# Kernel optimization log

Hardware: AMD Instinct MI355X
Metric: run time of the kernel (lower is better)

Reference implementation:

```python
import jax, jax.numpy as jnp
import numpy as np

N = 100000   # nodes
E = 3200000  # edges (avg degree 32)
D = 128      # in_channels
H = 128      # hidden_channels
A, S, ETH = 3, 2, 3  # head output dims


def _w(k, o, i):
    return jax.random.normal(k, (o, i), dtype=jnp.float32) / np.sqrt(i).astype(np.float32)


def setup_inputs() -> dict:
    key = jax.random.key(0)
    ks = jax.random.split(key, 20)
    x = jax.random.normal(ks[0], (N, D), dtype=jnp.float32)
    edge_index = jax.random.randint(ks[1], (2, E), 0, N, dtype=jnp.int64)
    inp = {"x": x, "edge_index": edge_index}
    # SAGEConv params: Wl applied to mean-aggregated neighbors, Wr to root, plus bias
    dims = [("1", D, H), ("2", H, H), ("3", H, H), ("a", H, A), ("s", H, S), ("e", H, ETH)]
    ki = 2
    for tag, i, o in dims:
        inp[f"W{tag}l"] = _w(ks[ki], o, i); ki += 1
        inp[f"W{tag}r"] = _w(ks[ki], o, i); ki += 1
        inp[f"b{tag}"] = jnp.zeros((o,), dtype=jnp.float32)
    return inp


def _sage(x, src, dst, inv_deg, Wl, Wr, b):
    # mean aggregation of source features onto destination nodes, then linear
    agg = jax.ops.segment_sum(x[src], dst, num_segments=N) * inv_deg  # [N, d]
    return agg @ Wl.T + x @ Wr.T + b


def reference(x, edge_index,
              W1l, W1r, b1, W2l, W2r, b2, W3l, W3r, b3,
              Wal, War, ba, Wsl, Wsr, bs, Wel, Wer, be):
    src, dst = edge_index[0], edge_index[1]
    deg = jax.ops.segment_sum(jnp.ones((E,), jnp.float32), dst, num_segments=N)
    inv_deg = (1.0 / jnp.maximum(deg, 1.0))[:, None]  # [N,1]
    h = jax.nn.relu(_sage(x, src, dst, inv_deg, W1l, W1r, b1))
    h = jax.nn.relu(_sage(h, src, dst, inv_deg, W2l, W2r, b2))
    h = jax.nn.relu(_sage(h, src, dst, inv_deg, W3l, W3r, b3))
    age_out = _sage(h, src, dst, inv_deg, Wal, War, ba)
    sex_out = _sage(h, src, dst, inv_deg, Wsl, Wsr, bs)
    eth_out = _sage(h, src, dst, inv_deg, Wel, Wer, be)
    return (age_out, sex_out, eth_out)
```

## Files before the change

kernel.cpp:

```cpp
#include <hip/hip_runtime.h>

#define TPB 256
#define NB1 256
#define NBUCK 512

using half4_t = __attribute__((ext_vector_type(4))) _Float16;
using half8_t = __attribute__((ext_vector_type(8))) _Float16;
using f32x4 = __attribute__((ext_vector_type(4))) float;


__global__ __launch_bounds__(256) void hist1_k(const int* __restrict__ ei,
                                               int* __restrict__ hist, int E, int stripe) {
  __shared__ int h[NBUCK];
  for (int i = threadIdx.x; i < NBUCK; i += 256) h[i] = 0;
  __syncthreads();
  int b0 = blockIdx.x * stripe;
  int b1 = min(b0 + stripe, E);
  for (int e = b0 + threadIdx.x; e < b1; e += 256) atomicAdd(&h[ei[E + e] >> 8], 1);
  __syncthreads();
  for (int i = threadIdx.x; i < NBUCK; i += 256) hist[i * NB1 + blockIdx.x] = h[i];
}

__global__ void scan1_k(const int* __restrict__ src, int* __restrict__ out,
                        int* __restrict__ chunk, int n) {
  __shared__ int sh[TPB];
  int i = blockIdx.x * TPB + threadIdx.x;
  int v = (i < n) ? src[i] : 0;
  sh[threadIdx.x] = v;
  __syncthreads();
  for (int off = 1; off < TPB; off <<= 1) {
    int t = (threadIdx.x >= off) ? sh[threadIdx.x - off] : 0;
    __syncthreads();
    sh[threadIdx.x] += t;
    __syncthreads();
  }
  if (i < n) out[i] = sh[threadIdx.x] - v;
  if (threadIdx.x == TPB - 1) chunk[blockIdx.x] = sh[TPB - 1];
}

__global__ void scan2_k(int* __restrict__ chunk, int nb) {
  __shared__ int sh[512];
  int v = (threadIdx.x < nb) ? chunk[threadIdx.x] : 0;
  sh[threadIdx.x] = v;
  __syncthreads();
  for (int off = 1; off < 512; off <<= 1) {
    int t = (threadIdx.x >= off) ? sh[threadIdx.x - off] : 0;
    __syncthreads();
    sh[threadIdx.x] += t;
    __syncthreads();
  }
  if (threadIdx.x < nb) chunk[threadIdx.x] = sh[threadIdx.x] - v;
}

__global__ void scan3_k(int* __restrict__ out, const int* __restrict__ chunk, int n) {
  int i = blockIdx.x * TPB + threadIdx.x;
  if (i < n) out[i] += chunk[blockIdx.x];
}

__global__ __launch_bounds__(256) void scatter1_k(const int* __restrict__ ei,
                                                  const int* __restrict__ base,
                                                  unsigned* __restrict__ ebuf, int E,
                                                  int stripe) {
  __shared__ int cur[NBUCK];
  for (int i = threadIdx.x; i < NBUCK; i += 256) cur[i] = base[i * NB1 + blockIdx.x];
  __syncthreads();
  int b0 = blockIdx.x * stripe;
  int b1 = min(b0 + stripe, E);
  for (int e = b0 + threadIdx.x; e < b1; e += 256) {
    int s = ei[e];
    int d = ei[E + e];
    int p = atomicAdd(&cur[d >> 8], 1);
    ebuf[p] = (unsigned)s | ((unsigned)(d & 255) << 24);
  }
}

__global__ __launch_bounds__(256) void build_k(const unsigned* __restrict__ ebuf,
                                               const int* __restrict__ base,
                                               int* __restrict__ row_start,
                                               int* __restrict__ deg,
                                               float* __restrict__ invd,
                                               int* __restrict__ csr, int N, int E) {
  __shared__ int h[256];
  __shared__ int excl[256];
  __shared__ int bse[2];
  int b = blockIdx.x;
  int t = threadIdx.x;
  if (t == 0) {
    bse[0] = base[b * NB1];
    bse[1] = (b + 1 < NBUCK) ? base[(b + 1) * NB1] : E;
  }
  h[t] = 0;
  __syncthreads();
  int bs = bse[0], be = bse[1];
  for (int e = bs + t; e < be; e += 256) atomicAdd(&h[ebuf[e] >> 24], 1);
  __syncthreads();
  int v = h[t];
  excl[t] = v;
  __syncthreads();
  for (int off = 1; off < 256; off <<= 1) {
    int tv = (t >= off) ? excl[t - off] : 0;
    __syncthreads();
    excl[t] += tv;
    __syncthreads();
  }
  int ex = excl[t] - v;
  int node = b * 256 + t;
  if (node < N) {
    row_start[node] = bs + ex;
    deg[node] = v;
    invd[node] = 1.0f / fmaxf((float)v, 1.0f);
  }
  h[t] = bs + ex;
  __syncthreads();
  for (int e = bs + t; e < be; e += 256) {
    unsigned p = ebuf[e];
    int pos = atomicAdd(&h[p >> 24], 1);
    csr[pos] = (int)(p & 0xFFFFFFu);
  }
}


__global__ void f2h_k(const float* __restrict__ in, _Float16* __restrict__ out, int n4) {
  int i = blockIdx.x * TPB + threadIdx.x;
  if (i < n4) {
    float4 v = ((const float4*)in)[i];
    half4_t o;
    o.x = (_Float16)v.x; o.y = (_Float16)v.y; o.z = (_Float16)v.z; o.w = (_Float16)v.w;
    ((half4_t*)out)[i] = o;
  }
}

__global__ void w6_k(const float* __restrict__ w0, const float* __restrict__ w1,
                     const float* __restrict__ w2, const float* __restrict__ w3,
                     const float* __restrict__ w4, const float* __restrict__ w5,
                     _Float16* __restrict__ out) {
  int t = blockIdx.x * TPB + threadIdx.x;
  if (t >= 6 * 4096) return;
  int which = t >> 12, i = t & 4095;
  const float* src = which == 0 ? w0 : which == 1 ? w1 : which == 2 ? w2
                   : which == 3 ? w3 : which == 4 ? w4 : w5;
  float4 v = ((const float4*)src)[i];
  half4_t o;
  o.x = (_Float16)v.x; o.y = (_Float16)v.y; o.z = (_Float16)v.z; o.w = (_Float16)v.w;
  ((half4_t*)out)[(size_t)which * 4096 + i] = o;
}


__global__ __launch_bounds__(256) void agg128_k(const _Float16* __restrict__ hb,
                                                const int* __restrict__ csr,
                                                const int* __restrict__ row_start,
                                                const int* __restrict__ deg,
                                                const float* __restrict__ invd,
                                                _Float16* __restrict__ out, int n) {
  int node = (blockIdx.x << 2) + (threadIdx.x >> 6);
  if (node >= n) return;
  int lane = threadIdx.x & 63;
  int g = lane >> 4;
  int l = lane & 15;
  int s = row_start[node];
  int c = deg[node];
  const _Float16* base = hb + (l << 3);
  float a0 = 0.f, a1 = 0.f, a2 = 0.f, a3 = 0.f;
  float a4 = 0.f, a5 = 0.f, a6 = 0.f, a7 = 0.f;
  int j = 0;
  if (c >= 16) {
    int id[4];
#pragma unroll
    for (int p = 0; p < 4; ++p) id[p] = csr[s + 4 * p + g];
    while (true) {
      half8_t v[4];
#pragma unroll
      for (int p = 0; p < 4; ++p) v[p] = *(const half8_t*)&base[(size_t)id[p] * 128];
      j += 16;
      bool more = (j + 16 <= c);
      if (more) {
#pragma unroll
        for (int p = 0; p < 4; ++p) id[p] = csr[s + j + 4 * p + g];
      }
#pragma unroll
      for (int p = 0; p < 4; ++p) {
        a0 += (float)v[p][0]; a1 += (float)v[p][1];
        a2 += (float)v[p][2]; a3 += (float)v[p][3];
        a4 += (float)v[p][4]; a5 += (float)v[p][5];
        a6 += (float)v[p][6]; a7 += (float)v[p][7];
      }
      if (!more) break;
    }
  }
  if (j < c) {
    int cm1 = c - 1;
#pragma unroll
    for (int p = 0; p < 4; ++p) {
      int e = j + 4 * p + g;
      float m = (e < c) ? 1.f : 0.f;
      int id = csr[s + min(e, cm1)];
      half8_t v = *(const half8_t*)&base[(size_t)id * 128];
      a0 = fmaf(m, (float)v[0], a0); a1 = fmaf(m, (float)v[1], a1);
      a2 = fmaf(m, (float)v[2], a2); a3 = fmaf(m, (float)v[3], a3);
      a4 = fmaf(m, (float)v[4], a4); a5 = fmaf(m, (float)v[5], a5);
      a6 = fmaf(m, (float)v[6], a6); a7 = fmaf(m, (float)v[7], a7);
    }
  }
  a0 += __shfl_xor(a0, 16); a1 += __shfl_xor(a1, 16);
  a2 += __shfl_xor(a2, 16); a3 += __shfl_xor(a3, 16);
  a4 += __shfl_xor(a4, 16); a5 += __shfl_xor(a5, 16);
  a6 += __shfl_xor(a6, 16); a7 += __shfl_xor(a7, 16);
  a0 += __shfl_xor(a0, 32); a1 += __shfl_xor(a1, 32);
  a2 += __shfl_xor(a2, 32); a3 += __shfl_xor(a3, 32);
  a4 += __shfl_xor(a4, 32); a5 += __shfl_xor(a5, 32);
  a6 += __shfl_xor(a6, 32); a7 += __shfl_xor(a7, 32);
  if (g == 0) {
    float w = invd[node];
    half8_t r;
    r[0] = (_Float16)(a0 * w); r[1] = (_Float16)(a1 * w);
    r[2] = (_Float16)(a2 * w); r[3] = (_Float16)(a3 * w);
    r[4] = (_Float16)(a4 * w); r[5] = (_Float16)(a5 * w);
    r[6] = (_Float16)(a6 * w); r[7] = (_Float16)(a7 * w);
    *(half8_t*)&out[(size_t)node * 128 + (l << 3)] = r;
  }
}


__global__ __launch_bounds__(256) void gemm2_k(
    const _Float16* __restrict__ Aagg, const _Float16* __restrict__ Ah,
    const _Float16* __restrict__ Wh,
    const float* __restrict__ bias, _Float16* __restrict__ outh, int n, int do_relu) {
  int wave = threadIdx.x >> 6;
  int lane = threadIdx.x & 63;
  int quad = lane >> 4;
  int l16 = lane & 15;
  int m0 = blockIdx.x * 64 + wave * 16;
  int arow = m0 + l16;
  bool valid = arow < n;
  size_t abase = (size_t)arow * 128 + quad * 8;

  f32x4 acc[8];
#pragma unroll
  for (int c = 0; c < 8; ++c) acc[c] = (f32x4){0.f, 0.f, 0.f, 0.f};

#pragma unroll
  for (int s = 0; s < 2; ++s) {
    const _Float16* A = s ? Ah : Aagg;
    const _Float16* W = Wh + (size_t)s * 16384;
#pragma unroll
    for (int kb = 0; kb < 128; kb += 32) {
      half8_t af;
      if (valid) {
        af = *(const half8_t*)&A[abase + kb];
      } else {
#pragma unroll
        for (int jj = 0; jj < 8; ++jj) af[jj] = (_Float16)0;
      }
#pragma unroll
      for (int c = 0; c < 8; ++c) {
        half8_t bf = *(const half8_t*)&W[(size_t)(c * 16 + l16) * 128 + kb + quad * 8];
        acc[c] = __builtin_amdgcn_mfma_f32_16x16x32_f16(af, bf, acc[c], 0, 0, 0);
      }
    }
  }

#pragma unroll
  for (int c = 0; c < 8; ++c) {
    float bcol = bias[c * 16 + l16];
#pragma unroll
    for (int r = 0; r < 4; ++r) {
      int row = m0 + quad * 4 + r;
      if (row < n) {
        float v = acc[c][r] + bcol;
        if (do_relu) v = fmaxf(v, 0.f);
        outh[(size_t)row * 128 + c * 16 + l16] = (_Float16)v;
      }
    }
  }
}


__global__ void pack_head_k(const float* __restrict__ Wal, const float* __restrict__ War,
                            const float* __restrict__ ba, const float* __restrict__ Wsl,
                            const float* __restrict__ Wsr, const float* __restrict__ bsx,
                            const float* __restrict__ Wel, const float* __restrict__ Wer,
                            const float* __restrict__ be, _Float16* __restrict__ Wcat,
                            float* __restrict__ bcat) {
  int t = blockIdx.x * TPB + threadIdx.x;
  float v = 0.f;
  bool ok = t < 2048;
  if (t < 384) v = Wal[t];
  else if (t < 640) v = Wsl[t - 384];
  else if (t < 1024) v = Wel[t - 640];
  else if (t < 1408) v = War[t - 1024];
  else if (t < 1664) v = Wsr[t - 1408];
  else if (t < 2048) v = Wer[t - 1664];
  if (ok) Wcat[t] = (_Float16)v;
  if (t < 16) {
    float b = 0.f;
    if (t >= 8 && t < 11) b = ba[t - 8];
    else if (t >= 11 && t < 13) b = bsx[t - 11];
    else if (t >= 13) b = be[t - 13];
    bcat[t] = b;
  }
}


__global__ __launch_bounds__(256) void head_gemm_k(const _Float16* __restrict__ h,
                                                   const _Float16* __restrict__ Wcat,
                                                   const float* __restrict__ bcat,
                                                   float* __restrict__ out_lr, int n) {
  __shared__ float hs[64 * 132];
  __shared__ float Ws[16 * 128];
  __shared__ float bsh[16];
  int tid = threadIdx.x;
  int m0 = blockIdx.x * 64;
  {
    half8_t w = *(const half8_t*)&Wcat[tid * 8];
#pragma unroll
    for (int jj = 0; jj < 8; ++jj) Ws[tid * 8 + jj] = (float)w[jj];
    if (tid < 16) bsh[tid] = bcat[tid];
  }
  {
    int row = tid >> 2, q = tid & 3;
    int grow = m0 + row;
#pragma unroll
    for (int j = 0; j < 4; ++j) {
      half8_t v;
      if (grow < n) {
        v = *(const half8_t*)&h[(size_t)grow * 128 + q * 32 + j * 8];
      } else {
#pragma unroll
        for (int jj = 0; jj < 8; ++jj) v[jj] = (_Float16)0;
      }
#pragma unroll
      for (int jj = 0; jj < 8; ++jj) hs[row * 132 + q * 32 + j * 8 + jj] = (float)v[jj];
    }
  }
  __syncthreads();
  int row = tid & 63, og = tid >> 6;
  float acc[4] = {0.f, 0.f, 0.f, 0.f};
#pragma unroll
  for (int k4 = 0; k4 < 32; ++k4) {
    float4 hv = *(float4*)&hs[row * 132 + k4 * 4];
#pragma unroll
    for (int i = 0; i < 4; ++i) {
      float4 wv = *(float4*)&Ws[(og * 4 + i) * 128 + k4 * 4];
      acc[i] += hv.x * wv.x + hv.y * wv.y + hv.z * wv.z + hv.w * wv.w;
    }
  }
  int grow = m0 + row;
  if (grow < n) {
#pragma unroll
    for (int i = 0; i < 4; ++i)
      out_lr[(size_t)grow * 16 + og * 4 + i] = acc[i] + bsh[og * 4 + i];
  }
}


__global__ void agg8_k(const float* __restrict__ hlr, const int* __restrict__ csr,
                       const int* __restrict__ row_start, const int* __restrict__ deg,
                       const float* __restrict__ invd, float* __restrict__ out, int n) {
  int node = (blockIdx.x << 2) + (threadIdx.x >> 6);
  if (node >= n) return;
  int lane = threadIdx.x & 63;
  int c2 = lane & 3;
  int g = lane >> 2;
  int s = row_start[node], cnt = deg[node];
  float ax = 0.f, ay = 0.f;
  int j = 0;
  for (; j + 32 <= cnt; j += 32) {
#pragma unroll
    for (int p = 0; p < 2; ++p) {
      int id = csr[s + j + 16 * p + g];
      float2 v = *(const float2*)&hlr[(size_t)id * 16 + 2 * c2];
      ax += v.x;
      ay += v.y;
    }
  }
  if (j < cnt) {
    int cm1 = cnt - 1;
#pragma unroll
    for (int p = 0; p < 2; ++p) {
      int e = j + 16 * p + g;
      float m = (e < cnt) ? 1.f : 0.f;
      int id = csr[s + min(e, cm1)];
      float2 v = *(const float2*)&hlr[(size_t)id * 16 + 2 * c2];
      ax = fmaf(m, v.x, ax);
      ay = fmaf(m, v.y, ay);
    }
  }
  ax += __shfl_xor(ax, 4);  ay += __shfl_xor(ay, 4);
  ax += __shfl_xor(ax, 8);  ay += __shfl_xor(ay, 8);
  ax += __shfl_xor(ax, 16); ay += __shfl_xor(ay, 16);
  ax += __shfl_xor(ax, 32); ay += __shfl_xor(ay, 32);
  if (g == 0) {
    float w = invd[node];
    float r0 = ax * w + hlr[(size_t)node * 16 + 8 + 2 * c2];
    float r1 = ay * w + hlr[(size_t)node * 16 + 8 + 2 * c2 + 1];
    float rr[2] = {r0, r1};
#pragma unroll
    for (int q = 0; q < 2; ++q) {
      int f = 2 * c2 + q;
      float r = rr[q];
      if (f < 3) out[(size_t)node * 3 + f] = r;
      else if (f < 5) out[(size_t)3 * n + (size_t)node * 2 + (f - 3)] = r;
      else out[(size_t)5 * n + (size_t)node * 3 + (f - 5)] = r;
    }
  }
}


extern "C" void kernel_launch(void* const* d_in, const int* in_sizes, int n_in,
                              void* d_out, int out_size, void* d_ws, size_t ws_size,
                              hipStream_t stream) {
  const float* x = (const float*)d_in[0];
  const int* ei = (const int*)d_in[1];
  const float* W1l = (const float*)d_in[2];
  const float* W1r = (const float*)d_in[3];
  const float* b1 = (const float*)d_in[4];
  const float* W2l = (const float*)d_in[5];
  const float* W2r = (const float*)d_in[6];
  const float* b2 = (const float*)d_in[7];
  const float* W3l = (const float*)d_in[8];
  const float* W3r = (const float*)d_in[9];
  const float* b3 = (const float*)d_in[10];
  const float* Wal = (const float*)d_in[11];
  const float* War = (const float*)d_in[12];
  const float* ba = (const float*)d_in[13];
  const float* Wsl = (const float*)d_in[14];
  const float* Wsr = (const float*)d_in[15];
  const float* bsx = (const float*)d_in[16];
  const float* Wel = (const float*)d_in[17];
  const float* Wer = (const float*)d_in[18];
  const float* be = (const float*)d_in[19];

  int N = in_sizes[0] / 128;
  int E = in_sizes[1] / 2;
  int NBKT = (N + 255) >> 8;

  char* w = (char*)d_ws;
  auto alloc = [&](size_t b) {
    char* p = w;
    w += (b + 255) & ~(size_t)255;
    return p;
  };
  int* deg = (int*)alloc((size_t)N * 4);
  int* row_start = (int*)alloc((size_t)N * 4);
  float* invd = (float*)alloc((size_t)N * 4);
  int* hist = (int*)alloc((size_t)NBUCK * NB1 * 4);
  int* chunk = (int*)alloc(512 * 4);
  int* csr = (int*)alloc((size_t)E * 4);
  size_t xh_bytes = (size_t)N * 128 * 2;
  size_t ebuf_bytes = (size_t)E * 4;
  char* region = (char*)alloc(xh_bytes > ebuf_bytes ? xh_bytes : ebuf_bytes);
  unsigned* ebuf = (unsigned*)region;
  _Float16* xh = (_Float16*)region;
  _Float16* aggh = (_Float16*)alloc((size_t)N * 128 * 2);
  _Float16* hA = (_Float16*)alloc((size_t)N * 128 * 2);
  _Float16* hB = (_Float16*)alloc((size_t)N * 128 * 2);
  _Float16* wh = (_Float16*)alloc((size_t)6 * 16384 * 2);
  _Float16* Wcat = (_Float16*)alloc(2048 * 2);
  float* bcat = (float*)alloc(16 * 4);
  float* head_lr = (float*)alloc((size_t)N * 16 * 4);

  int stripe = (((E + NB1 - 1) / NB1) + 255) & ~255;
  int nscan = NBUCK * NB1;
  int nbScan = (nscan + TPB - 1) / TPB;
  int nbNode = (N + 3) / 4;
  int nbM = (N + 63) / 64;
  int nbC = (N * 32 + TPB - 1) / TPB;

  hist1_k<<<NB1, 256, 0, stream>>>(ei, hist, E, stripe);
  scan1_k<<<nbScan, TPB, 0, stream>>>(hist, hist, chunk, nscan);
  scan2_k<<<1, 512, 0, stream>>>(chunk, nbScan);
  scan3_k<<<nbScan, TPB, 0, stream>>>(hist, chunk, nscan);
  scatter1_k<<<NB1, 256, 0, stream>>>(ei, hist, ebuf, E, stripe);
  build_k<<<NBKT, 256, 0, stream>>>(ebuf, hist, row_start, deg, invd, csr, N, E);

  f2h_k<<<nbC, TPB, 0, stream>>>(x, xh, N * 32);
  w6_k<<<96, TPB, 0, stream>>>(W1l, W1r, W2l, W2r, W3l, W3r, wh);
  pack_head_k<<<8, TPB, 0, stream>>>(Wal, War, ba, Wsl, Wsr, bsx, Wel, Wer, be, Wcat, bcat);

  agg128_k<<<nbNode, TPB, 0, stream>>>(xh, csr, row_start, deg, invd, aggh, N);
  gemm2_k<<<nbM, TPB, 0, stream>>>(aggh, xh, wh + 0 * 16384, b1, hA, N, 1);
  agg128_k<<<nbNode, TPB, 0, stream>>>(hA, csr, row_start, deg, invd, aggh, N);
  gemm2_k<<<nbM, TPB, 0, stream>>>(aggh, hA, wh + 2 * 16384, b2, hB, N, 1);
  agg128_k<<<nbNode, TPB, 0, stream>>>(hB, csr, row_start, deg, invd, aggh, N);
  gemm2_k<<<nbM, TPB, 0, stream>>>(aggh, hB, wh + 4 * 16384, b3, hA, N, 1);
  head_gemm_k<<<nbM, TPB, 0, stream>>>(hA, Wcat, bcat, head_lr, N);
  agg8_k<<<nbNode, TPB, 0, stream>>>(head_lr, csr, row_start, deg, invd, (float*)d_out, N);
}
```

Measured before the change: 798.8 us.

## Stage weights in swizzled LDS, MFMA head GEMM, merge prep kernels, split head buffer

The three prep kernels (x conversion, layer-weight conversion, head-weight packing) become one launch. gemm2_k now preloads its A fragments and stages the 64 KB fp16 weight matrix in XOR-swizzled LDS instead of re-reading it from global per MFMA. head_gemm_k replaces its fp32 LDS dot-product loop with a 16x16x32 MFMA. The head output is split into separate neighbour and root buffers so agg8 gathers 32-byte rows instead of 64-byte rows. The 64 KB of LDS per block in gemm2 may cap occupancy, and each block pays a full weight copy.

```diff
diff --git a/kernel.cpp b/kernel.cpp
--- a/kernel.cpp
+++ b/kernel.cpp
@@ -120,29 +120,50 @@
 }
 
 
-__global__ void f2h_k(const float* __restrict__ in, _Float16* __restrict__ out, int n4) {
-  int i = blockIdx.x * TPB + threadIdx.x;
-  if (i < n4) {
-    float4 v = ((const float4*)in)[i];
+__global__ void prep_k(const float* __restrict__ x, _Float16* __restrict__ xh, int n4,
+                       const float* __restrict__ w0, const float* __restrict__ w1,
+                       const float* __restrict__ w2, const float* __restrict__ w3,
+                       const float* __restrict__ w4, const float* __restrict__ w5,
+                       _Float16* __restrict__ wh,
+                       const float* __restrict__ Wal, const float* __restrict__ War,
+                       const float* __restrict__ ba, const float* __restrict__ Wsl,
+                       const float* __restrict__ Wsr, const float* __restrict__ bsx,
+                       const float* __restrict__ Wel, const float* __restrict__ Wer,
+                       const float* __restrict__ be, _Float16* __restrict__ Wcat,
+                       float* __restrict__ bcat) {
+  int t = blockIdx.x * TPB + threadIdx.x;
+  if (t < n4) {
+    float4 v = ((const float4*)x)[t];
     half4_t o;
     o.x = (_Float16)v.x; o.y = (_Float16)v.y; o.z = (_Float16)v.z; o.w = (_Float16)v.w;
-    ((half4_t*)out)[i] = o;
-  }
-}
-
-__global__ void w6_k(const float* __restrict__ w0, const float* __restrict__ w1,
-                     const float* __restrict__ w2, const float* __restrict__ w3,
-                     const float* __restrict__ w4, const float* __restrict__ w5,
-                     _Float16* __restrict__ out) {
-  int t = blockIdx.x * TPB + threadIdx.x;
-  if (t >= 6 * 4096) return;
-  int which = t >> 12, i = t & 4095;
-  const float* src = which == 0 ? w0 : which == 1 ? w1 : which == 2 ? w2
-                   : which == 3 ? w3 : which == 4 ? w4 : w5;
-  float4 v = ((const float4*)src)[i];
-  half4_t o;
-  o.x = (_Float16)v.x; o.y = (_Float16)v.y; o.z = (_Float16)v.z; o.w = (_Float16)v.w;
-  ((half4_t*)out)[(size_t)which * 4096 + i] = o;
+    ((half4_t*)xh)[t] = o;
+  }
+  if (t < 6 * 4096) {
+    int which = t >> 12, i = t & 4095;
+    const float* src = which == 0 ? w0 : which == 1 ? w1 : which == 2 ? w2
+                     : which == 3 ? w3 : which == 4 ? w4 : w5;
+    float4 v = ((const float4*)src)[i];
+    half4_t o;
+    o.x = (_Float16)v.x; o.y = (_Float16)v.y; o.z = (_Float16)v.z; o.w = (_Float16)v.w;
+    ((half4_t*)wh)[(size_t)which * 4096 + i] = o;
+  }
+  if (t < 2048) {
+    float v = 0.f;
+    if (t < 384) v = Wal[t];
+    else if (t < 640) v = Wsl[t - 384];
+    else if (t < 1024) v = Wel[t - 640];
+    else if (t < 1408) v = War[t - 1024];
+    else if (t < 1664) v = Wsr[t - 1408];
+    else v = Wer[t - 1664];
+    Wcat[t] = (_Float16)v;
+  }
+  if (t < 16) {
+    float b = 0.f;
+    if (t >= 8 && t < 11) b = ba[t - 8];
+    else if (t >= 11 && t < 13) b = bsx[t - 11];
+    else if (t >= 13) b = be[t - 13];
+    bcat[t] = b;
+  }
 }
 
 
@@ -224,79 +245,77 @@
 __global__ __launch_bounds__(256) void gemm2_k(
     const _Float16* __restrict__ Aagg, const _Float16* __restrict__ Ah,
     const _Float16* __restrict__ Wh,
-    const float* __restrict__ bias, _Float16* __restrict__ outh, int n, int do_relu) {
-  int wave = threadIdx.x >> 6;
-  int lane = threadIdx.x & 63;
-  int quad = lane >> 4;
-  int l16 = lane & 15;
+    const float* __restrict__ bias, _Float16* __restrict__ outh, int n) {
+  __shared__ _Float16 Ws[32768];
+  int tid = threadIdx.x;
+  int wave = tid >> 6;
+  int lane = tid & 63;
+  int g = lane >> 4;
+  int l = lane & 15;
   int m0 = blockIdx.x * 64 + wave * 16;
-  int arow = m0 + l16;
+  int arow = m0 + l;
   bool valid = arow < n;
-  size_t abase = (size_t)arow * 128 + quad * 8;
+
+  half8_t afA[4], afH[4];
+  size_t abase = (size_t)arow * 128 + g * 8;
+  if (valid) {
+#pragma unroll
+    for (int kb = 0; kb < 4; ++kb) afA[kb] = *(const half8_t*)&Aagg[abase + kb * 32];
+#pragma unroll
+    for (int kb = 0; kb < 4; ++kb) afH[kb] = *(const half8_t*)&Ah[abase + kb * 32];
+  } else {
+#pragma unroll
+    for (int kb = 0; kb < 4; ++kb) {
+#pragma unroll
+      for (int jj = 0; jj < 8; ++jj) { afA[kb][jj] = (_Float16)0; afH[kb][jj] = (_Float16)0; }
+    }
+  }
+
+#pragma unroll
+  for (int it = 0; it < 16; ++it) {
+    int ci = tid + it * 256;
+    int row = ci >> 4;
+    int kc = ci & 15;
+    float4 v = *(const float4*)&Wh[(size_t)row * 128 + kc * 8];
+    *(float4*)&Ws[(size_t)row * 128 + ((kc ^ (row & 7)) * 8)] = v;
+  }
+  __syncthreads();
 
   f32x4 acc[8];
 #pragma unroll
-  for (int c = 0; c < 8; ++c) acc[c] = (f32x4){0.f, 0.f, 0.f, 0.f};
-
-#pragma unroll
-  for (int s = 0; s < 2; ++s) {
-    const _Float16* A = s ? Ah : Aagg;
-    const _Float16* W = Wh + (size_t)s * 16384;
-#pragma unroll
-    for (int kb = 0; kb < 128; kb += 32) {
-      half8_t af;
-      if (valid) {
-        af = *(const half8_t*)&A[abase + kb];
-      } else {
-#pragma unroll
-        for (int jj = 0; jj < 8; ++jj) af[jj] = (_Float16)0;
+  for (int ct = 0; ct < 8; ++ct) acc[ct] = (f32x4){0.f, 0.f, 0.f, 0.f};
+
+#pragma unroll
+  for (int kb = 0; kb < 4; ++kb) {
+#pragma unroll
+    for (int ct = 0; ct < 8; ++ct) {
+      int row = ct * 16 + l;
+      half8_t bf = *(const half8_t*)&Ws[(size_t)row * 128 + (((kb * 4 + g) ^ (l & 7)) * 8)];
+      acc[ct] = __builtin_amdgcn_mfma_f32_16x16x32_f16(afA[kb], bf, acc[ct], 0, 0, 0);
+    }
+  }
+#pragma unroll
+  for (int kb = 0; kb < 4; ++kb) {
+#pragma unroll
+    for (int ct = 0; ct < 8; ++ct) {
+      int row = 128 + ct * 16 + l;
+      half8_t bf = *(const half8_t*)&Ws[(size_t)row * 128 + (((kb * 4 + g) ^ (l & 7)) * 8)];
+      acc[ct] = __builtin_amdgcn_mfma_f32_16x16x32_f16(afH[kb], bf, acc[ct], 0, 0, 0);
+    }
+  }
+
+#pragma unroll
+  for (int ct = 0; ct < 8; ++ct) {
+    int col = ct * 16 + l;
+    float bc = bias[col];
+#pragma unroll
+    for (int r = 0; r < 4; ++r) {
+      int row = m0 + g * 4 + r;
+      if (row < n) {
+        float v = fmaxf(acc[ct][r] + bc, 0.f);
+        outh[(size_t)row * 128 + col] = (_Float16)v;
       }
-#pragma unroll
-      for (int c = 0; c < 8; ++c) {
-        half8_t bf = *(const half8_t*)&W[(size_t)(c * 16 + l16) * 128 + kb + quad * 8];
-        acc[c] = __builtin_amdgcn_mfma_f32_16x16x32_f16(af, bf, acc[c], 0, 0, 0);
-      }
-    }
-  }
-
-#pragma unroll
-  for (int c = 0; c < 8; ++c) {
-    float bcol = bias[c * 16 + l16];
-#pragma unroll
-    for (int r = 0; r < 4; ++r) {
-      int row = m0 + quad * 4 + r;
-      if (row < n) {
-        float v = acc[c][r] + bcol;
-        if (do_relu) v = fmaxf(v, 0.f);
-        outh[(size_t)row * 128 + c * 16 + l16] = (_Float16)v;
-      }
-    }
-  }
-}
-
-
-__global__ void pack_head_k(const float* __restrict__ Wal, const float* __restrict__ War,
-                            const float* __restrict__ ba, const float* __restrict__ Wsl,
-                            const float* __restrict__ Wsr, const float* __restrict__ bsx,
-                            const float* __restrict__ Wel, const float* __restrict__ Wer,
-                            const float* __restrict__ be, _Float16* __restrict__ Wcat,
-                            float* __restrict__ bcat) {
-  int t = blockIdx.x * TPB + threadIdx.x;
-  float v = 0.f;
-  bool ok = t < 2048;
-  if (t < 384) v = Wal[t];
-  else if (t < 640) v = Wsl[t - 384];
-  else if (t < 1024) v = Wel[t - 640];
-  else if (t < 1408) v = War[t - 1024];
-  else if (t < 1664) v = Wsr[t - 1408];
-  else if (t < 2048) v = Wer[t - 1664];
-  if (ok) Wcat[t] = (_Float16)v;
-  if (t < 16) {
-    float b = 0.f;
-    if (t >= 8 && t < 11) b = ba[t - 8];
-    else if (t >= 11 && t < 13) b = bsx[t - 11];
-    else if (t >= 13) b = be[t - 13];
-    bcat[t] = b;
+    }
   }
 }
 
@@ -304,58 +323,56 @@
 __global__ __launch_bounds__(256) void head_gemm_k(const _Float16* __restrict__ h,
                                                    const _Float16* __restrict__ Wcat,
                                                    const float* __restrict__ bcat,
-                                                   float* __restrict__ out_lr, int n) {
-  __shared__ float hs[64 * 132];
-  __shared__ float Ws[16 * 128];
-  __shared__ float bsh[16];
+                                                   float* __restrict__ head_g,
+                                                   float* __restrict__ head_r, int n) {
+  __shared__ _Float16 Ws[2048];
+  __shared__ float bs[16];
   int tid = threadIdx.x;
-  int m0 = blockIdx.x * 64;
   {
-    half8_t w = *(const half8_t*)&Wcat[tid * 8];
-#pragma unroll
-    for (int jj = 0; jj < 8; ++jj) Ws[tid * 8 + jj] = (float)w[jj];
-    if (tid < 16) bsh[tid] = bcat[tid];
-  }
-  {
-    int row = tid >> 2, q = tid & 3;
-    int grow = m0 + row;
-#pragma unroll
-    for (int j = 0; j < 4; ++j) {
-      half8_t v;
-      if (grow < n) {
-        v = *(const half8_t*)&h[(size_t)grow * 128 + q * 32 + j * 8];
-      } else {
-#pragma unroll
-        for (int jj = 0; jj < 8; ++jj) v[jj] = (_Float16)0;
-      }
-#pragma unroll
-      for (int jj = 0; jj < 8; ++jj) hs[row * 132 + q * 32 + j * 8 + jj] = (float)v[jj];
-    }
-  }
-  __syncthreads();
-  int row = tid & 63, og = tid >> 6;
-  float acc[4] = {0.f, 0.f, 0.f, 0.f};
-#pragma unroll
-  for (int k4 = 0; k4 < 32; ++k4) {
-    float4 hv = *(float4*)&hs[row * 132 + k4 * 4];
-#pragma unroll
-    for (int i = 0; i < 4; ++i) {
-      float4 wv = *(float4*)&Ws[(og * 4 + i) * 128 + k4 * 4];
-      acc[i] += hv.x * wv.x + hv.y * wv.y + hv.z * wv.z + hv.w * wv.w;
-    }
-  }
-  int grow = m0 + row;
-  if (grow < n) {
-#pragma unroll
-    for (int i = 0; i < 4; ++i)
-      out_lr[(size_t)grow * 16 + og * 4 + i] = acc[i] + bsh[og * 4 + i];
-  }
-}
-
-
-__global__ void agg8_k(const float* __restrict__ hlr, const int* __restrict__ csr,
-                       const int* __restrict__ row_start, const int* __restrict__ deg,
-                       const float* __restrict__ invd, float* __restrict__ out, int n) {
+    int row = tid >> 4, kc = tid & 15;
+    float4 v = *(const float4*)&Wcat[(size_t)row * 128 + kc * 8];
+    *(float4*)&Ws[(size_t)row * 128 + ((kc ^ (row & 7)) * 8)] = v;
+    if (tid < 16) bs[tid] = bcat[tid];
+  }
+  __syncthreads();
+  int wave = tid >> 6;
+  int lane = tid & 63;
+  int g = lane >> 4;
+  int l = lane & 15;
+  int m0 = blockIdx.x * 64 + wave * 16;
+  int arow = m0 + l;
+  bool valid = arow < n;
+  size_t abase = (size_t)arow * 128 + g * 8;
+  f32x4 acc = (f32x4){0.f, 0.f, 0.f, 0.f};
+#pragma unroll
+  for (int kb = 0; kb < 4; ++kb) {
+    half8_t af;
+    if (valid) {
+      af = *(const half8_t*)&h[abase + kb * 32];
+    } else {
+#pragma unroll
+      for (int jj = 0; jj < 8; ++jj) af[jj] = (_Float16)0;
+    }
+    half8_t bf = *(const half8_t*)&Ws[(size_t)l * 128 + (((kb * 4 + g) ^ (l & 7)) * 8)];
+    acc = __builtin_amdgcn_mfma_f32_16x16x32_f16(af, bf, acc, 0, 0, 0);
+  }
+  float bc = bs[l];
+#pragma unroll
+  for (int r = 0; r < 4; ++r) {
+    int row = m0 + g * 4 + r;
+    if (row < n) {
+      float v = acc[r] + bc;
+      if (l < 8) head_g[(size_t)row * 8 + l] = v;
+      else head_r[(size_t)row * 8 + (l - 8)] = v;
+    }
+  }
+}
+
+
+__global__ void agg8_k(const float* __restrict__ head_g, const float* __restrict__ head_r,
+                       const int* __restrict__ csr, const int* __restrict__ row_start,
+                       const int* __restrict__ deg, const float* __restrict__ invd,
+                       float* __restrict__ out, int n) {
   int node = (blockIdx.x << 2) + (threadIdx.x >> 6);
   if (node >= n) return;
   int lane = threadIdx.x & 63;
@@ -368,7 +385,7 @@
 #pragma unroll
     for (int p = 0; p < 2; ++p) {
       int id = csr[s + j + 16 * p + g];
-      float2 v = *(const float2*)&hlr[(size_t)id * 16 + 2 * c2];
+      float2 v = *(const float2*)&head_g[(size_t)id * 8 + 2 * c2];
       ax += v.x;
       ay += v.y;
     }
@@ -380,7 +397,7 @@
       int e = j + 16 * p + g;
       float m = (e < cnt) ? 1.f : 0.f;
       int id = csr[s + min(e, cm1)];
-      float2 v = *(const float2*)&hlr[(size_t)id * 16 + 2 * c2];
+      float2 v = *(const float2*)&head_g[(size_t)id * 8 + 2 * c2];
       ax = fmaf(m, v.x, ax);
       ay = fmaf(m, v.y, ay);
     }
@@ -391,8 +408,8 @@
   ax += __shfl_xor(ax, 32); ay += __shfl_xor(ay, 32);
   if (g == 0) {
     float w = invd[node];
-    float r0 = ax * w + hlr[(size_t)node * 16 + 8 + 2 * c2];
-    float r1 = ay * w + hlr[(size_t)node * 16 + 8 + 2 * c2 + 1];
+    float r0 = ax * w + head_r[(size_t)node * 8 + 2 * c2];
+    float r1 = ay * w + head_r[(size_t)node * 8 + 2 * c2 + 1];
     float rr[2] = {r0, r1};
 #pragma unroll
     for (int q = 0; q < 2; ++q) {
@@ -457,7 +474,8 @@
   _Float16* wh = (_Float16*)alloc((size_t)6 * 16384 * 2);
   _Float16* Wcat = (_Float16*)alloc(2048 * 2);
   float* bcat = (float*)alloc(16 * 4);
-  float* head_lr = (float*)alloc((size_t)N * 16 * 4);
+  float* head_g = (float*)alloc((size_t)N * 8 * 4);
+  float* head_r = (float*)alloc((size_t)N * 8 * 4);
 
   int stripe = (((E + NB1 - 1) / NB1) + 255) & ~255;
   int nscan = NBUCK * NB1;
@@ -473,16 +491,16 @@
   scatter1_k<<<NB1, 256, 0, stream>>>(ei, hist, ebuf, E, stripe);
   build_k<<<NBKT, 256, 0, stream>>>(ebuf, hist, row_start, deg, invd, csr, N, E);
 
-  f2h_k<<<nbC, TPB, 0, stream>>>(x, xh, N * 32);
-  w6_k<<<96, TPB, 0, stream>>>(W1l, W1r, W2l, W2r, W3l, W3r, wh);
-  pack_head_k<<<8, TPB, 0, stream>>>(Wal, War, ba, Wsl, Wsr, bsx, Wel, Wer, be, Wcat, bcat);
+  prep_k<<<nbC, TPB, 0, stream>>>(x, xh, N * 32, W1l, W1r, W2l, W2r, W3l, W3r, wh,
+                                  Wal, War, ba, Wsl, Wsr, bsx, Wel, Wer, be, Wcat, bcat);
 
   agg128_k<<<nbNode, TPB, 0, stream>>>(xh, csr, row_start, deg, invd, aggh, N);
-  gemm2_k<<<nbM, TPB, 0, stream>>>(aggh, xh, wh + 0 * 16384, b1, hA, N, 1);
+  gemm2_k<<<nbM, TPB, 0, stream>>>(aggh, xh, wh + 0 * 16384, b1, hA, N);
   agg128_k<<<nbNode, TPB, 0, stream>>>(hA, csr, row_start, deg, invd, aggh, N);
-  gemm2_k<<<nbM, TPB, 0, stream>>>(aggh, hA, wh + 2 * 16384, b2, hB, N, 1);
+  gemm2_k<<<nbM, TPB, 0, stream>>>(aggh, hA, wh + 2 * 16384, b2, hB, N);
   agg128_k<<<nbNode, TPB, 0, stream>>>(hB, csr, row_start, deg, invd, aggh, N);
-  gemm2_k<<<nbM, TPB, 0, stream>>>(aggh, hB, wh + 4 * 16384, b3, hA, N, 1);
-  head_gemm_k<<<nbM, TPB, 0, stream>>>(hA, Wcat, bcat, head_lr, N);
-  agg8_k<<<nbNode, TPB, 0, stream>>>(head_lr, csr, row_start, deg, invd, (float*)d_out, N);
-}
+  gemm2_k<<<nbM, TPB, 0, stream>>>(aggh, hB, wh + 4 * 16384, b3, hA, N);
+  head_gemm_k<<<nbM, TPB, 0, stream>>>(hA, Wcat, bcat, head_g, head_r, N);
+  agg8_k<<<nbNode, TPB, 0, stream>>>(head_g, head_r, csr, row_start, deg, invd,
+                                     (float*)d_out, N);
+}
```

After: 681.4 us. -14.7%, faster.
